# Kernel optimization log

Hardware: AMD Instinct MI355X
Metric: run time of the kernel (lower is better)

The kernel has to match this reference:

```python
import jax, jax.numpy as jnp
import numpy as np
from jax import lax

B, S, H, W = 8, 8, 256, 256  # batch, split_num, crop_size, crop_size


def _sn(w, seed):
    # spectral norm, 1 power iteration, u/v detached (torch spectral_norm semantics)
    o = w.shape[0]
    m = w.reshape(o, -1)
    u = jnp.asarray(np.random.RandomState(seed).randn(o).astype(np.float32))
    u = u / (jnp.linalg.norm(u) + 1e-12)
    v = m.T @ u
    v = v / (jnp.linalg.norm(v) + 1e-12)
    u2 = m @ v
    u2 = u2 / (jnp.linalg.norm(u2) + 1e-12)
    u2 = lax.stop_gradient(u2)
    v = lax.stop_gradient(v)
    sigma = u2 @ (m @ v)
    return w / sigma


def _conv(x, w, stride, groups):
    return lax.conv_general_dilated(x, w, (stride, stride), ((1, 1), (1, 1)),
                                    feature_group_count=groups,
                                    dimension_numbers=('NCHW', 'OIHW', 'NCHW'))


def _inorm(x):
    # InstanceNorm2d(affine=False, eps=1e-5)
    m = x.mean((2, 3), keepdims=True)
    v = ((x - m) ** 2).mean((2, 3), keepdims=True)
    return (x - m) * lax.rsqrt(v + 1e-5)


def _lrelu(x):
    return jnp.where(x >= 0, x, 0.2 * x)


def _crop_resize(img, mask):
    # img [3,H,W], mask [H,W]: mask, bbox of nonzero support, nearest-resize crop to (H,W)
    seg = img * mask
    c = seg.sum(0)
    col = c.sum(0)   # y_seg, per-column sums [W]
    row = c.sum(1)   # x_seg, per-row sums [H]
    cnz = col != 0
    rnz = row != 0
    ok = jnp.any(cnz) & jnp.any(rnz)
    y0 = jnp.argmax(cnz)
    y1 = W - 1 - jnp.argmax(cnz[::-1])
    x0 = jnp.argmax(rnz)
    x1 = H - 1 - jnp.argmax(rnz[::-1])
    h = x1 - x0 + 1
    w = y1 - y0 + 1
    # torch F.interpolate nearest: src = floor(dst * in / out)
    r = x0 + (jnp.arange(H) * h) // H
    cc = y0 + (jnp.arange(W) * w) // W
    resized = seg[:, r[:, None], cc[None, :]]
    return jnp.where(ok, resized, seg)


def _trans_img(real_image, semantic):
    f = jax.vmap(lambda img, masks: jax.vmap(lambda m: _crop_resize(img, m))(masks))
    imgs = f(real_image, semantic)            # [B,S,3,H,W]
    return imgs.reshape(B, S * 3, H, W)


def _forward(real_image, input_semantic, w1, w2, w3, w4, w5, w6, gw1, gb1, gw2, gb2):
    images = _trans_img(real_image, input_semantic)
    a = _lrelu
    x = _inorm(_conv(images, _sn(w1, 1), 2, S))          # [B,64,128,128]
    x = _inorm(_conv(a(x), _sn(w2, 2), 2, S))            # [B,128,64,64]
    out_8 = _inorm(_conv(a(x), _sn(w3, 3), 2, S))        # [B,256,32,32]
    out_16 = _inorm(_conv(a(out_8), _sn(w4, 4), 2, S))   # [B,512,16,16]
    out_32 = _inorm(_conv(a(out_16), _sn(w5, 5), 2, S))  # [B,1024,8,8]
    x = a(_inorm(_conv(a(out_32), _sn(w6, 6), 1, S)))    # [B,2048,8,8]
    x_1 = a(_conv(a(out_16), gw1, 1, 1) + gb1[None, :, None, None])  # [B,2048,16,16]
    x_2 = a(_conv(a(out_8), gw2, 1, 1) + gb2[None, :, None, None])   # [B,2048,32,32]
    return x, x_1, x_2, images


def setup_inputs() -> dict:
    key = jax.random.key(0)
    ks = jax.random.split(key, 12)
    real_image = jax.random.normal(ks[0], (B, 3, H, W), jnp.float32)
    input_semantic = jax.random.randint(ks[1], (B, S, H, W), 0, 2).astype(jnp.float32)
    def cw(k, o, i, kk=3):
        return jax.random.normal(k, (o, i, kk, kk), jnp.float32) * 0.05
    return {
        'real_image': real_image,
        'input_semantic': input_semantic,
        'w1': cw(ks[2], 64, 3),
        'w2': cw(ks[3], 128, 8),
        'w3': cw(ks[4], 256, 16),
        'w4': cw(ks[5], 512, 32),
        'w5': cw(ks[6], 1024, 64),
        'w6': cw(ks[7], 2048, 128),
        'gw1': cw(ks[8], 2048, 512, 1),
        'gb1': jnp.zeros((2048,), jnp.float32),
        'gw2': cw(ks[9], 2048, 256, 1),
        'gb2': jnp.zeros((2048,), jnp.float32),
    }


def reference(real_image, input_semantic, w1, w2, w3, w4, w5, w6, gw1, gb1, gw2, gb2):
    return _forward(real_image, input_semantic, w1, w2, w3, w4, w5, w6, gw1, gb1, gw2, gb2)
```

## Files before the change

kernel.cpp:

```cpp
#include <hip/hip_runtime.h>
#include <math.h>

#define WS_OFF_U     0
#define WS_OFF_T     4096
#define WS_OFF_TN    6400
#define WS_OFF_S2    6408
#define WS_OFF_BBOX  6416
#define WS_OFF_W     8192
#define WS_OFF_C     3152896
#define WS_OFF_D     5250048

#define OUT_X    0
#define OUT_X1   1048576
#define OUT_X2   6356992
#define OUT_IMG  25296896

struct Ptr6 { const float* p[6]; };

typedef short s16x8 __attribute__((ext_vector_type(8)));
typedef float f32x4 __attribute__((ext_vector_type(4)));
typedef unsigned int u32x4 __attribute__((ext_vector_type(4)));

#define MT_UP 0x80000000u
#define MT_LO 0x7fffffffu

__global__ __launch_bounds__(256) void gen_u_par(float* ws){
  const int os[6]   = {64,128,256,512,1024,2048};
  const int uoff[6] = {0,64,192,448,960,1984};
  int l = blockIdx.x;
  int n = os[l];
  int tid = threadIdx.x;

  __shared__ unsigned mt[624];
  __shared__ unsigned draws[8192];
  __shared__ float px[2048], py[2048];
  __shared__ unsigned char accf[2048];
  __shared__ int scan[256];

  if (tid == 0){
    unsigned seed = (unsigned)(l + 1);
    for (int i = 0; i < 624; i++){
      mt[i] = seed;
      seed = 1812433253u * (seed ^ (seed >> 30)) + (unsigned)(i + 1);
    }
  }
  __syncthreads();

  int need = 4 * n;
  int twists = (need + 623) / 624;
  for (int t = 0; t < twists; t++){
    unsigned yA = 0, vA = 0;
    if (tid < 227){ yA = (mt[tid] & MT_UP) | (mt[tid+1] & MT_LO); vA = mt[tid+397]; }
    __syncthreads();
    if (tid < 227){ mt[tid] = vA ^ (yA >> 1) ^ ((yA & 1u) ? 0x9908b0dfu : 0u); }
    __syncthreads();
    unsigned yB = 0, vB = 0; int iB = 227 + tid;
    if (tid < 227){ yB = (mt[iB] & MT_UP) | (mt[iB+1] & MT_LO); vB = mt[iB-227]; }
    __syncthreads();
    if (tid < 227){ mt[iB] = vB ^ (yB >> 1) ^ ((yB & 1u) ? 0x9908b0dfu : 0u); }
    __syncthreads();
    unsigned yC = 0, vC = 0; int iC = 454 + tid;
    if (tid < 169){ yC = (mt[iC] & MT_UP) | (mt[iC+1] & MT_LO); vC = mt[iC-227]; }
    __syncthreads();
    if (tid < 169){ mt[iC] = vC ^ (yC >> 1) ^ ((yC & 1u) ? 0x9908b0dfu : 0u); }
    __syncthreads();
    if (tid == 0){
      unsigned y = (mt[623] & MT_UP) | (mt[0] & MT_LO);
      mt[623] = mt[396] ^ (y >> 1) ^ ((y & 1u) ? 0x9908b0dfu : 0u);
    }
    __syncthreads();
    for (int i = tid; i < 624; i += 256){
      int pos = t * 624 + i;
      if (pos < need){
        unsigned y = mt[i];
        y ^= y >> 11; y ^= (y << 7) & 0x9d2c5680u; y ^= (y << 15) & 0xefc60000u; y ^= y >> 18;
        draws[pos] = y;
      }
    }
    __syncthreads();
  }

  int A = (n + 255) / 256;
  int local = 0;
  for (int a = 0; a < A; a++){
    int k = tid * A + a;
    if (k < n){
      double u1 = ((draws[4*k]   >> 5) * 67108864.0 + (draws[4*k+1] >> 6)) / 9007199254740992.0;
      double u2 = ((draws[4*k+2] >> 5) * 67108864.0 + (draws[4*k+3] >> 6)) / 9007199254740992.0;
      double x1 = 2.0*u1 - 1.0, x2 = 2.0*u2 - 1.0;
      double r2 = x1*x1 + x2*x2;
      int ok = (r2 < 1.0 && r2 != 0.0);
      accf[k] = (unsigned char)ok;
      if (ok){
        double f = sqrt(-2.0 * log(r2) / r2);
        px[k] = (float)(f * x2);
        py[k] = (float)(f * x1);
      }
      local += ok;
    }
  }
  scan[tid] = local;
  __syncthreads();
  if (tid == 0){
    int run = 0;
    for (int i = 0; i < 256; i++){ int c = scan[i]; scan[i] = run; run += c; }
  }
  __syncthreads();
  int j = scan[tid];
  float* u = ws + WS_OFF_U + uoff[l];
  for (int a = 0; a < A; a++){
    int k = tid * A + a;
    if (k < n && accf[k]){
      if (2*j + 1 < n){ u[2*j] = px[k]; u[2*j+1] = py[k]; }
      j++;
    }
  }
}

__global__ __launch_bounds__(256) void sn_t_kernel(Ptr6 wp, float* ws){
  const int cols[6] = {27,72,144,288,576,1152};
  const int uoff[6] = {0,64,192,448,960,1984};
  const int toff[6] = {0,27,99,243,531,1107};
  const int cstart[7] = {0,4,12,28,60,124,252};
  int b = blockIdx.x;
  int l = 0; while (l < 5 && b >= cstart[l+1]) l++;
  int chunk = b - cstart[l];
  int r0 = chunk * 16;
  int C = cols[l];
  const float* m = wp.p[l];
  const float* u = ws + WS_OFF_U + uoff[l];
  float* t = ws + WS_OFF_T + toff[l];
  __shared__ float us[16];
  if (threadIdx.x < 16) us[threadIdx.x] = u[r0 + threadIdx.x];
  __syncthreads();
  for (int j = threadIdx.x; j < C; j += 256){
    float acc = 0.f;
    #pragma unroll
    for (int r = 0; r < 16; r++) acc += m[(size_t)(r0 + r) * C + j] * us[r];
    atomicAdd(&t[j], acc);
  }
}

__global__ void sn_tn_kernel(float* ws){
  const int cols[6] = {27,72,144,288,576,1152};
  const int toff[6] = {0,27,99,243,531,1107};
  int l = blockIdx.x;
  const float* t = ws + WS_OFF_T + toff[l];
  float s = 0.f;
  for (int j = threadIdx.x; j < cols[l]; j += 256){ float v = t[j]; s += v*v; }
  __shared__ float sb[4];
  int lane = threadIdx.x & 63, wid = threadIdx.x >> 6;
  for (int o = 32; o; o >>= 1) s += __shfl_down(s, o, 64);
  if (lane == 0) sb[wid] = s;
  __syncthreads();
  if (threadIdx.x == 0) ws[WS_OFF_TN + l] = sb[0] + sb[1] + sb[2] + sb[3];
}

__global__ __launch_bounds__(256) void sn_z_kernel(Ptr6 wp, float* ws){
  const int cols[6] = {27,72,144,288,576,1152};
  const int toff[6] = {0,27,99,243,531,1107};
  const int rstart[7] = {0,64,192,448,960,1984,4032};
  __shared__ float part[6];
  if (threadIdx.x < 6) part[threadIdx.x] = 0.f;
  __syncthreads();
  int gr = blockIdx.x * 4 + (threadIdx.x >> 6);
  int lane = threadIdx.x & 63;
  if (gr < 4032){
    int l = 0; while (l < 5 && gr >= rstart[l+1]) l++;
    int row = gr - rstart[l];
    int C = cols[l];
    const float* m = wp.p[l] + (size_t)row * C;
    const float* t = ws + WS_OFF_T + toff[l];
    float acc = 0.f;
    for (int c = lane; c < C; c += 64) acc += m[c] * t[c];
    for (int o = 32; o; o >>= 1) acc += __shfl_down(acc, o, 64);
    if (lane == 0) atomicAdd(&part[l], acc * acc);
  }
  __syncthreads();
  if (threadIdx.x < 6 && part[threadIdx.x] != 0.f)
    atomicAdd(&ws[WS_OFF_S2 + threadIdx.x], part[threadIdx.x]);
}

__global__ void wscale_kernel(const float* __restrict__ src, float* __restrict__ dst,
                              int n, const float* __restrict__ tn, const float* __restrict__ s2){
  int i = blockIdx.x * 256 + threadIdx.x;
  if (i >= n) return;
  float inv = sqrtf(tn[0] / s2[0]);
  dst[i] = src[i] * inv;
}

__global__ __launch_bounds__(256) void bbox_stage1(const float* __restrict__ img,
                                                   const float* __restrict__ sem,
                                                   int* __restrict__ colpart,
                                                   int* __restrict__ rowflag){
  int chunk = blockIdx.x;
  int s = blockIdx.y;
  int b = blockIdx.z;
  int w = threadIdx.x;
  int h0 = chunk * 32;
  const float* i0 = img + (size_t)(b*3 + 0) * 65536;
  const float* i1 = i0 + 65536;
  const float* i2 = i1 + 65536;
  const float* mk = sem + (size_t)(b*8 + s) * 65536;
  __shared__ int rflags[32];
  if (w < 32) rflags[w] = 0;
  __syncthreads();
  int lane = w & 63;
  int myflag = 0;
  #pragma unroll 4
  for (int r = 0; r < 32; r++){
    int off = (h0 + r)*256 + w;
    float v = (i0[off] + i1[off] + i2[off]) * mk[off];
    int nz = (v != 0.f);
    myflag |= nz;
    unsigned long long bal = __ballot(nz);
    if (lane == 0 && bal) rflags[r] = 1;
  }
  __syncthreads();
  int bs = b*8 + s;
  colpart[(bs*8 + chunk)*256 + w] = myflag;
  if (w < 32) rowflag[bs*256 + h0 + w] = rflags[w];
}

__global__ __launch_bounds__(256) void bbox_stage2(const int* __restrict__ colpart,
                                                   const int* __restrict__ rowflag,
                                                   int* __restrict__ bbox){
  int bs = blockIdx.x;
  int w = threadIdx.x;
  int colnz = 0;
  #pragma unroll
  for (int c = 0; c < 8; c++) colnz |= colpart[(bs*8 + c)*256 + w];
  int rownz = rowflag[bs*256 + w];
  __shared__ int red[256];
  red[w] = colnz ? w : 256; __syncthreads();
  for (int st = 128; st; st >>= 1){ if (w < st) red[w] = min(red[w], red[w+st]); __syncthreads(); }
  int y0 = red[0]; __syncthreads();
  red[w] = colnz ? w : -1; __syncthreads();
  for (int st = 128; st; st >>= 1){ if (w < st) red[w] = max(red[w], red[w+st]); __syncthreads(); }
  int y1 = red[0]; __syncthreads();
  red[w] = rownz ? w : 256; __syncthreads();
  for (int st = 128; st; st >>= 1){ if (w < st) red[w] = min(red[w], red[w+st]); __syncthreads(); }
  int x0 = red[0]; __syncthreads();
  red[w] = rownz ? w : -1; __syncthreads();
  for (int st = 128; st; st >>= 1){ if (w < st) red[w] = max(red[w], red[w+st]); __syncthreads(); }
  int x1 = red[0];
  if (w == 0){
    int ok = (y0 < 256) && (x0 < 256);
    int base = bs * 4;
    bbox[base+0] = ok ? x0 : 0;
    bbox[base+1] = ok ? (x1 - x0 + 1) : 256;
    bbox[base+2] = ok ? y0 : 0;
    bbox[base+3] = ok ? (y1 - y0 + 1) : 256;
  }
}

__global__ void transimg_kernel(const float* __restrict__ img, const float* __restrict__ sem,
                                const int* __restrict__ bbox, float* __restrict__ out){
  int idx = blockIdx.x * 256 + threadIdx.x;
  int j = idx & 255;
  int i = (idx >> 8) & 255;
  int c = idx >> 16;
  int b = c / 24, ch24 = c % 24;
  int s = ch24 / 3, ch = ch24 % 3;
  const int* bb = bbox + (b*8 + s) * 4;
  int ri = bb[0] + ((i * bb[1]) >> 8);
  int cj = bb[2] + ((j * bb[3]) >> 8);
  float m = sem[((size_t)(b*8 + s) * 256 + ri) * 256 + cj];
  float v = img[((size_t)(b*3 + ch) * 256 + ri) * 256 + cj];
  out[idx] = v * m;
}

template<int CIN_G, int CIN_CHUNK, int COUT_G, int OCC, int RELU_IN>
__global__ __launch_bounds__(256) void conv3x3_tile(const float* __restrict__ in,
                                                    const float* __restrict__ wt,
                                                    float* __restrict__ out,
                                                    int Hin, int Hout){
  constexpr int TIH = 65, TIW = 65, RS = 66;
  constexpr int NOC = COUT_G / OCC;
  constexpr int NSTAGE = CIN_G / CIN_CHUNK;
  __shared__ float xs[CIN_CHUNK][TIH][RS];
  __shared__ float wsh[OCC][CIN_CHUNK*9];
  int tid = threadIdx.x;
  int g = blockIdx.y, b = blockIdx.z;
  int ocChunk = blockIdx.x % NOC;
  int tileId  = blockIdx.x / NOC;
  int tilesX = Hout >> 5;
  int tileX = tileId % tilesX, tileY = tileId / tilesX;
  int oh0 = tileY*32, ow0 = tileX*32;
  int ih0 = oh0*2 - 1, iw0 = ow0*2 - 1;
  int sx = tid & 15, sy = tid >> 4;
  const int Cin_tot = CIN_G*8;

  float acc[OCC][2][2];
  #pragma unroll
  for (int o = 0; o < OCC; o++)
    #pragma unroll
    for (int i2 = 0; i2 < 2; i2++)
      #pragma unroll
      for (int j2 = 0; j2 < 2; j2++) acc[o][i2][j2] = 0.f;

  for (int st = 0; st < NSTAGE; st++){
    int icb = st*CIN_CHUNK;
    for (int i = tid; i < CIN_CHUNK*TIH*TIW; i += 256){
      int ic = i / (TIH*TIW);
      int rem = i - ic*(TIH*TIW);
      int r = rem / TIW, c = rem - r*TIW;
      int ih = ih0 + r, iw = iw0 + c;
      float v = 0.f;
      if ((unsigned)ih < (unsigned)Hin && (unsigned)iw < (unsigned)Hin){
        v = in[((size_t)(b*Cin_tot + g*CIN_G + icb + ic)*Hin + ih)*Hin + iw];
        if (RELU_IN) v = (v >= 0.f) ? v : 0.2f*v;
      }
      xs[ic][r][c] = v;
    }
    for (int i = tid; i < OCC*CIN_CHUNK*9; i += 256){
      int o = i / (CIN_CHUNK*9);
      int rr = i - o*(CIN_CHUNK*9);
      int ic = rr / 9, tap = rr - ic*9;
      wsh[o][rr] = wt[((size_t)(g*COUT_G + ocChunk*OCC + o)*CIN_G + icb + ic)*9 + tap];
    }
    __syncthreads();
    #pragma unroll
    for (int ic = 0; ic < CIN_CHUNK; ic++){
      #pragma unroll
      for (int kh = 0; kh < 3; kh++){
        #pragma unroll
        for (int kw = 0; kw < 3; kw++){
          float wv[OCC];
          #pragma unroll
          for (int o = 0; o < OCC; o++) wv[o] = wsh[o][ic*9 + kh*3 + kw];
          #pragma unroll
          for (int i2 = 0; i2 < 2; i2++){
            #pragma unroll
            for (int j2 = 0; j2 < 2; j2++){
              float x = xs[ic][2*(sy + 16*i2) + kh][2*(sx + 16*j2) + kw];
              #pragma unroll
              for (int o = 0; o < OCC; o++) acc[o][i2][j2] += wv[o]*x;
            }
          }
        }
      }
    }
    if (st + 1 < NSTAGE) __syncthreads();
  }

  #pragma unroll
  for (int o = 0; o < OCC; o++){
    int oc = g*COUT_G + ocChunk*OCC + o;
    #pragma unroll
    for (int i2 = 0; i2 < 2; i2++)
      #pragma unroll
      for (int j2 = 0; j2 < 2; j2++){
        int oh = oh0 + sy + 16*i2, ow = ow0 + sx + 16*j2;
        out[((size_t)(b*COUT_G*8 + oc)*Hout + oh)*Hout + ow] = acc[o][i2][j2];
      }
  }
}

template<int STRIDE, int CIN_G, int COUT_G, int HSH>
__global__ __launch_bounds__(256) void conv3x3_gemm(const float* __restrict__ in,
                                                    const float* __restrict__ wt,
                                                    float* __restrict__ out,
                                                    int Hin){
  constexpr int K = CIN_G*9;
  const int Hout = 1 << HSH;
  int z = blockIdx.z; int b = z >> 3, g = z & 7;
  int n0 = blockIdx.x * 64, oc0 = blockIdx.y * 64;
  __shared__ float Ws[16][68];
  __shared__ float Xs[16][68];
  int tid = threadIdx.x;
  int tx = tid & 15, ty = tid >> 4;
  int pixl = tid & 63;
  int kkb = (tid >> 6) << 2;
  float acc[4][4];
  #pragma unroll
  for (int i = 0; i < 4; i++)
    #pragma unroll
    for (int j = 0; j < 4; j++) acc[i][j] = 0.f;

  for (int k0 = 0; k0 < K; k0 += 16){
    #pragma unroll
    for (int r = 0; r < 4; r++){
      int oc_l = (tid >> 4) + 16*r;
      int kk = tid & 15;
      Ws[kk][oc_l] = wt[((size_t)(g*COUT_G + oc0 + oc_l))*K + k0 + kk];
    }
    #pragma unroll
    for (int r = 0; r < 4; r++){
      int kk = kkb + r;
      int k = k0 + kk;
      int ic = k / 9, tap = k - ic*9;
      int dh = tap / 3, dw = tap - dh*3;
      int n = n0 + pixl;
      int oh = n >> HSH, ow = n & (Hout - 1);
      int ih = oh*STRIDE - 1 + dh, iw = ow*STRIDE - 1 + dw;
      float v = 0.f;
      if ((unsigned)ih < (unsigned)Hin && (unsigned)iw < (unsigned)Hin){
        v = in[((size_t)(b*CIN_G*8 + g*CIN_G + ic)*Hin + ih)*Hin + iw];
        v = (v >= 0.f) ? v : 0.2f*v;
      }
      Xs[kk][pixl] = v;
    }
    __syncthreads();
    #pragma unroll
    for (int kk = 0; kk < 16; kk++){
      float4 wv = *(const float4*)&Ws[kk][ty*4];
      float4 xv = *(const float4*)&Xs[kk][tx*4];
      acc[0][0] += wv.x*xv.x; acc[0][1] += wv.x*xv.y; acc[0][2] += wv.x*xv.z; acc[0][3] += wv.x*xv.w;
      acc[1][0] += wv.y*xv.x; acc[1][1] += wv.y*xv.y; acc[1][2] += wv.y*xv.z; acc[1][3] += wv.y*xv.w;
      acc[2][0] += wv.z*xv.x; acc[2][1] += wv.z*xv.y; acc[2][2] += wv.z*xv.z; acc[2][3] += wv.z*xv.w;
      acc[3][0] += wv.w*xv.x; acc[3][1] += wv.w*xv.y; acc[3][2] += wv.w*xv.z; acc[3][3] += wv.w*xv.w;
    }
    __syncthreads();
  }

  #pragma unroll
  for (int i = 0; i < 4; i++){
    int oc = g*COUT_G + oc0 + ty*4 + i;
    #pragma unroll
    for (int j = 0; j < 4; j++){
      int n = n0 + tx*4 + j;
      int oh = n >> HSH, ow = n & (Hout - 1);
      out[((size_t)(b*COUT_G*8 + oc)*Hout + oh)*Hout + ow] = acc[i][j];
    }
  }
}

__global__ void inorm_kernel(const float* __restrict__ in, float* __restrict__ out,
                             int N, int relu_out){
  int bc = blockIdx.x;
  const float* p = in + (size_t)bc * N;
  float* q = out + (size_t)bc * N;
  float s = 0.f, ss = 0.f;
  for (int i = threadIdx.x; i < N; i += blockDim.x){ float x = p[i]; s += x; ss += x*x; }
  __shared__ float sb[8];
  int lane = threadIdx.x & 63, wid = threadIdx.x >> 6;
  for (int o = 32; o; o >>= 1){ s += __shfl_down(s, o, 64); ss += __shfl_down(ss, o, 64); }
  if (lane == 0){ sb[wid] = s; sb[4 + wid] = ss; }
  __syncthreads();
  if (threadIdx.x == 0){
    int nw = blockDim.x >> 6;
    float S = 0.f, SS = 0.f;
    for (int i = 0; i < nw; i++){ S += sb[i]; SS += sb[4+i]; }
    float mean = S / N;
    float var = SS / N - mean*mean;
    sb[0] = mean;
    sb[4] = rsqrtf(var + 1e-5f);
  }
  __syncthreads();
  float mean = sb[0], r = sb[4];
  for (int i = threadIdx.x; i < N; i += blockDim.x){
    float y = (p[i] - mean) * r;
    if (relu_out) y = (y >= 0.f) ? y : 0.2f*y;
    q[i] = y;
  }
}

template<int P>
__global__ void inorm_sum(const float* __restrict__ in, float* __restrict__ out,
                          int N, size_t pstride, int relu_out){
  int bc = blockIdx.x;
  const float* p = in + (size_t)bc * N;
  float* q = out + (size_t)bc * N;
  float s = 0.f, ss = 0.f;
  for (int i = threadIdx.x; i < N; i += blockDim.x){
    float x = 0.f;
    #pragma unroll
    for (int pp = 0; pp < P; pp++) x += p[(size_t)pp*pstride + i];
    q[i] = x;
    s += x; ss += x*x;
  }
  __shared__ float sb[8];
  int lane = threadIdx.x & 63, wid = threadIdx.x >> 6;
  for (int o = 32; o; o >>= 1){ s += __shfl_down(s, o, 64); ss += __shfl_down(ss, o, 64); }
  if (lane == 0){ sb[wid] = s; sb[4 + wid] = ss; }
  __syncthreads();
  if (threadIdx.x == 0){
    int nw = blockDim.x >> 6;
    float S = 0.f, SS = 0.f;
    for (int i = 0; i < nw; i++){ S += sb[i]; SS += sb[4+i]; }
    float mean = S / N;
    float var = SS / N - mean*mean;
    sb[0] = mean;
    sb[4] = rsqrtf(var + 1e-5f);
  }
  __syncthreads();
  float mean = sb[0], r = sb[4];
  for (int i = threadIdx.x; i < N; i += blockDim.x){
    float y = (q[i] - mean) * r;
    if (relu_out) y = (y >= 0.f) ? y : 0.2f*y;
    q[i] = y;
  }
}

__device__ __forceinline__ void split_bf16(float v, unsigned short& h, unsigned short& l){
  unsigned u = __float_as_uint(v);
  unsigned r = (u + 0x7FFFu + ((u >> 16) & 1u)) >> 16;
  h = (unsigned short)r;
  float hf = __uint_as_float(r << 16);
  float lo = v - hf;
  unsigned u2 = __float_as_uint(lo);
  unsigned r2 = (u2 + 0x7FFFu + ((u2 >> 16) & 1u)) >> 16;
  l = (unsigned short)r2;
}

template<int C, int HW>
__global__ __launch_bounds__(256) void cvt_x_kernel(const float* __restrict__ src,
                                                    unsigned short* __restrict__ dst){
  __shared__ float tile[64][65];
  int b = blockIdx.z;
  int c0 = blockIdx.y * 64, p0 = blockIdx.x * 64;
  const float* sp = src + ((size_t)b*C + c0)*HW + p0;
  for (int i = threadIdx.x; i < 64*64; i += 256){
    int ch = i >> 6, px = i & 63;
    float v = sp[(size_t)ch*HW + px];
    tile[ch][px] = (v >= 0.f) ? v : 0.2f*v;
  }
  __syncthreads();
  unsigned short* dp = dst + ((size_t)b*HW + p0)*(3*C) + c0;
  for (int i = threadIdx.x; i < 64*64; i += 256){
    int px = i >> 6, ch = i & 63;
    float v = tile[ch][px];
    unsigned short h, l; split_bf16(v, h, l);
    unsigned short* row = dp + (size_t)px*(3*C);
    row[ch] = h; row[C + ch] = l; row[2*C + ch] = h;
  }
}

template<int C>
__global__ __launch_bounds__(256) void cvt_w_kernel(const float* __restrict__ wt,
                                                    unsigned short* __restrict__ dst){
  int i = blockIdx.x * 256 + threadIdx.x;
  int oc = i / C, k = i & (C - 1);
  float v = wt[i];
  unsigned short h, l; split_bf16(v, h, l);
  unsigned short* row = dst + (size_t)oc * 3 * C;
  row[k] = h; row[C + k] = h; row[2*C + k] = l;
}

template<int K>
__global__ __launch_bounds__(256) void cvt_w_g(const float* __restrict__ wt,
                                               unsigned short* __restrict__ dst, int total){
  int i = blockIdx.x * 256 + threadIdx.x;
  if (i >= total) return;
  int oc = i / K, k = i - oc*K;
  float v = wt[i];
  unsigned short h, l; split_bf16(v, h, l);
  unsigned short* row = dst + (size_t)oc * 3 * K;
  row[k] = h; row[K + k] = h; row[2*K + k] = l;
}

template<int K, int K3PAD>
__global__ __launch_bounds__(256) void cvt_w_pad(const float* __restrict__ wt,
                                                 unsigned short* __restrict__ dst, int total){
  int i = blockIdx.x * 256 + threadIdx.x;
  if (i >= total) return;
  int oc = i / K3PAD, kk = i - oc*K3PAD;
  unsigned short o = 0;
  if (kk < 3*K){
    int which = kk / K, k = kk - which*K;
    float v = wt[(size_t)oc*K + k];
    unsigned short h, l; split_bf16(v, h, l);
    o = (which == 2) ? l : h;
  }
  dst[i] = o;
}

template<int CIN_G, int Hin, int STRIDE>
__global__ __launch_bounds__(256) void cvt_im2col(const float* __restrict__ in,
                                                  unsigned short* __restrict__ dst){
  constexpr int K = CIN_G*9;
  constexpr int K3 = 3*K;
  int g = blockIdx.x, b = blockIdx.y, pc = blockIdx.z;
  const float* src = in + (size_t)(b*CIN_G*8 + g*CIN_G)*Hin*Hin;
  unsigned short* drow = dst + ((size_t)g*512 + b*64 + pc*16)*K3;
  for (int idx = threadIdx.x; idx < 16*K; idx += 256){
    int pixl = idx / K, k = idx - pixl*K;
    int ic = k / 9, tap = k - ic*9;
    int dh = tap / 3, dw = tap - dh*3;
    int gp = pc*16 + pixl;
    int oh = gp >> 3, ow = gp & 7;
    int ih = oh*STRIDE - 1 + dh, iw = ow*STRIDE - 1 + dw;
    float v = 0.f;
    if ((unsigned)ih < (unsigned)Hin && (unsigned)iw < (unsigned)Hin){
      v = src[((size_t)ic*Hin + ih)*Hin + iw];
      v = (v >= 0.f) ? v : 0.2f*v;
    }
    unsigned short h, l; split_bf16(v, h, l);
    unsigned short* row = drow + (size_t)pixl*K3;
    row[k] = h; row[K + k] = l; row[2*K + k] = h;
  }
}

template<int CIN_G, int Hin, int HOSH, int STRIDE, int K3PAD, int NB>
__global__ __launch_bounds__(256) void cvt_im2col_g(const float* __restrict__ in,
                                                    unsigned short* __restrict__ dst, int b0){
  constexpr int K = CIN_G*9;
  constexpr int Hout = 1 << HOSH;
  constexpr int HW = Hout*Hout;
  int g = blockIdx.x, bl = blockIdx.y, pc = blockIdx.z;
  int b = b0 + bl;
  const float* src = in + (size_t)(b*CIN_G*8 + g*CIN_G)*Hin*Hin;
  unsigned short* drow = dst + ((size_t)g*(NB*HW) + (size_t)bl*HW + pc*64)*K3PAD;
  for (int idx = threadIdx.x; idx < 64*K; idx += 256){
    int pixl = idx / K, k = idx - pixl*K;
    int ic = k / 9, tap = k - ic*9;
    int dh = tap / 3, dw = tap - dh*3;
    int gp = pc*64 + pixl;
    int oh = gp >> HOSH, ow = gp & (Hout - 1);
    int ih = oh*STRIDE - 1 + dh, iw = ow*STRIDE - 1 + dw;
    float v = 0.f;
    if ((unsigned)ih < (unsigned)Hin && (unsigned)iw < (unsigned)Hin){
      v = src[((size_t)ic*Hin + ih)*Hin + iw];
      v = (v >= 0.f) ? v : 0.2f*v;
    }
    unsigned short h, l; split_bf16(v, h, l);
    unsigned short* row = drow + (size_t)pixl*K3PAD;
    row[k] = h; row[K + k] = l; row[2*K + k] = h;
  }
  for (int idx = threadIdx.x; idx < 64*(K3PAD - 3*K); idx += 256){
    int pixl = idx / (K3PAD - 3*K), k = idx - pixl*(K3PAD - 3*K);
    drow[(size_t)pixl*K3PAD + 3*K + k] = 0;
  }
}

template<int K3, int HW, int H>
__global__ __launch_bounds__(256) void conv1x1_mfma(const unsigned short* __restrict__ XT,
                                                    const unsigned short* __restrict__ WT,
                                                    const float* __restrict__ bias,
                                                    float* __restrict__ out){
  constexpr int Wp = H + 2;
  constexpr int NKT = K3 / 64;
  __shared__ unsigned short As[8*128*8];
  __shared__ unsigned short Bs[8*128*8];
  int tid = threadIdx.x;
  int b = blockIdx.z;
  int oc0 = blockIdx.y * 128;
  int px0 = blockIdx.x * 128;
  int lane = tid & 63;
  int wv = tid >> 6;
  int wy = wv >> 1, wx = wv & 1;

  int srow = tid >> 3;
  int sc8  = tid & 7;
  const unsigned short* Ag = WT + (size_t)(oc0 + srow)*K3 + sc8*8;
  const unsigned short* Bg = XT + ((size_t)b*HW + px0 + srow)*K3 + sc8*8;

  f32x4 acc[4][4];
  #pragma unroll
  for (int i = 0; i < 4; i++)
    #pragma unroll
    for (int j = 0; j < 4; j++) acc[i][j] = (f32x4){0.f,0.f,0.f,0.f};

  for (int kt = 0; kt < NKT; kt++){
    int k0 = kt * 64;
    #pragma unroll
    for (int q = 0; q < 4; q++){
      u32x4 av = *(const u32x4*)(Ag + (size_t)(32*q)*K3 + k0);
      u32x4 bv = *(const u32x4*)(Bg + (size_t)(32*q)*K3 + k0);
      *(u32x4*)&As[(sc8*128 + srow + 32*q)*8] = av;
      *(u32x4*)&Bs[(sc8*128 + srow + 32*q)*8] = bv;
    }
    __syncthreads();
    #pragma unroll
    for (int s = 0; s < 2; s++){
      int cb = s*4 + (lane >> 4);
      s16x8 af[4], bfr[4];
      #pragma unroll
      for (int mt = 0; mt < 4; mt++)
        af[mt] = *(const s16x8*)&As[(cb*128 + wy*64 + mt*16 + (lane & 15))*8];
      #pragma unroll
      for (int nt = 0; nt < 4; nt++)
        bfr[nt] = *(const s16x8*)&Bs[(cb*128 + wx*64 + nt*16 + (lane & 15))*8];
      #pragma unroll
      for (int mt = 0; mt < 4; mt++)
        #pragma unroll
        for (int nt = 0; nt < 4; nt++)
          acc[mt][nt] = __builtin_amdgcn_mfma_f32_16x16x32_bf16(af[mt], bfr[nt], acc[mt][nt], 0, 0, 0);
    }
    __syncthreads();
  }

  #pragma unroll
  for (int mt = 0; mt < 4; mt++){
    #pragma unroll
    for (int r = 0; r < 4; r++){
      int oc = oc0 + wy*64 + mt*16 + (lane >> 4)*4 + r;
      float bv2 = bias[oc];
      float* ob = out + ((size_t)b*2048 + oc)*Wp*Wp;
      #pragma unroll
      for (int nt = 0; nt < 4; nt++){
        int pix = px0 + wx*64 + nt*16 + (lane & 15);
        int ph = pix / H, pw2 = pix % H;
        float v = acc[mt][nt][r] + bv2;
        v = (v >= 0.f) ? v : 0.2f*v;
        ob[(size_t)(ph + 1)*Wp + pw2 + 1] = v;
      }
    }
  }
}

template<int K3, int COUT_G, int CTOT, int KSPLIT>
__global__ __launch_bounds__(256) void grouped_mfma(const unsigned short* __restrict__ XT,
                                                    const unsigned short* __restrict__ WT,
                                                    float* __restrict__ out, size_t pstride){
  constexpr int NKT = K3 / 64;
  constexpr int SPK = NKT / KSPLIT;
  __shared__ unsigned short As[8*128*8];
  __shared__ unsigned short Bs[8*128*8];
  int tid = threadIdx.x;
  int oc0 = blockIdx.y * 128;
  int g = oc0 / COUT_G;
  int px0 = blockIdx.x * 128;
  int ks = blockIdx.z;
  out += (size_t)ks * pstride;
  int lane = tid & 63;
  int wv = tid >> 6;
  int wy = wv >> 1, wx = wv & 1;

  int srow = tid >> 3;
  int sc8  = tid & 7;
  const unsigned short* Ag = WT + (size_t)(oc0 + srow)*K3 + sc8*8;
  const unsigned short* Bg = XT + ((size_t)g*512 + px0 + srow)*K3 + sc8*8;

  f32x4 acc[4][4];
  #pragma unroll
  for (int i = 0; i < 4; i++)
    #pragma unroll
    for (int j = 0; j < 4; j++) acc[i][j] = (f32x4){0.f,0.f,0.f,0.f};

  for (int kt = ks*SPK; kt < (ks+1)*SPK; kt++){
    int k0 = kt * 64;
    #pragma unroll
    for (int q = 0; q < 4; q++){
      u32x4 av = *(const u32x4*)(Ag + (size_t)(32*q)*K3 + k0);
      u32x4 bv = *(const u32x4*)(Bg + (size_t)(32*q)*K3 + k0);
      int rr = srow + 32*q;
      *(u32x4*)&As[(sc8*128 + (rr ^ sc8))*8] = av;
      *(u32x4*)&Bs[(sc8*128 + (rr ^ sc8))*8] = bv;
    }
    __syncthreads();
    #pragma unroll
    for (int s = 0; s < 2; s++){
      int cb = s*4 + (lane >> 4);
      s16x8 af[4], bfr[4];
      #pragma unroll
      for (int mt = 0; mt < 4; mt++){
        int row = wy*64 + mt*16 + (lane & 15);
        af[mt] = *(const s16x8*)&As[(cb*128 + (row ^ cb))*8];
      }
      #pragma unroll
      for (int nt = 0; nt < 4; nt++){
        int row = wx*64 + nt*16 + (lane & 15);
        bfr[nt] = *(const s16x8*)&Bs[(cb*128 + (row ^ cb))*8];
      }
      #pragma unroll
      for (int mt = 0; mt < 4; mt++)
        #pragma unroll
        for (int nt = 0; nt < 4; nt++)
          acc[mt][nt] = __builtin_amdgcn_mfma_f32_16x16x32_bf16(af[mt], bfr[nt], acc[mt][nt], 0, 0, 0);
    }
    __syncthreads();
  }

  #pragma unroll
  for (int mt = 0; mt < 4; mt++){
    #pragma unroll
    for (int r = 0; r < 4; r++){
      int oc = oc0 + wy*64 + mt*16 + (lane >> 4)*4 + r;
      #pragma unroll
      for (int nt = 0; nt < 4; nt++){
        int row = px0 + wx*64 + nt*16 + (lane & 15);
        int b = row >> 6, p = row & 63;
        out[((size_t)(b*CTOT + oc))*64 + p] = acc[mt][nt][r];
      }
    }
  }
}

template<int K3PAD, int COUT_G, int CTOT, int HW, int NROWS>
__global__ __launch_bounds__(256) void gconv_mfma(const unsigned short* __restrict__ XT,
                                                  const unsigned short* __restrict__ WT,
                                                  float* __restrict__ out, int b0){
  constexpr int NKT = K3PAD / 64;
  constexpr int MF = COUT_G / 16;
  __shared__ unsigned short As[8*COUT_G*8];
  __shared__ unsigned short Bs[8*128*8];
  int tid = threadIdx.x;
  int g = blockIdx.y;
  int px0 = blockIdx.x * 128;
  int lane = tid & 63;
  int wv = tid >> 6;

  int srow = tid >> 3;
  int sc8  = tid & 7;
  const unsigned short* Ag = WT + (size_t)(g*COUT_G + (srow & (COUT_G-1)))*K3PAD + sc8*8;
  const unsigned short* Bg = XT + ((size_t)g*NROWS + px0 + srow)*K3PAD + sc8*8;

  f32x4 acc[MF][2];
  #pragma unroll
  for (int i = 0; i < MF; i++)
    #pragma unroll
    for (int j = 0; j < 2; j++) acc[i][j] = (f32x4){0.f,0.f,0.f,0.f};

  for (int kt = 0; kt < NKT; kt++){
    int k0 = kt * 64;
    if (srow < COUT_G)
      *(u32x4*)&As[(sc8*COUT_G + srow)*8] = *(const u32x4*)(Ag + k0);
    #pragma unroll
    for (int q = 0; q < 4; q++)
      *(u32x4*)&Bs[(sc8*128 + srow + 32*q)*8] = *(const u32x4*)(Bg + (size_t)(32*q)*K3PAD + k0);
    __syncthreads();
    #pragma unroll
    for (int s = 0; s < 2; s++){
      int cb = s*4 + (lane >> 4);
      s16x8 af[MF], bfr[2];
      #pragma unroll
      for (int mt = 0; mt < MF; mt++)
        af[mt] = *(const s16x8*)&As[(cb*COUT_G + mt*16 + (lane & 15))*8];
      #pragma unroll
      for (int nt = 0; nt < 2; nt++)
        bfr[nt] = *(const s16x8*)&Bs[(cb*128 + wv*32 + nt*16 + (lane & 15))*8];
      #pragma unroll
      for (int mt = 0; mt < MF; mt++)
        #pragma unroll
        for (int nt = 0; nt < 2; nt++)
          acc[mt][nt] = __builtin_amdgcn_mfma_f32_16x16x32_bf16(af[mt], bfr[nt], acc[mt][nt], 0, 0, 0);
    }
    __syncthreads();
  }

  #pragma unroll
  for (int mt = 0; mt < MF; mt++){
    #pragma unroll
    for (int r = 0; r < 4; r++){
      int oc = g*COUT_G + mt*16 + (lane >> 4)*4 + r;
      #pragma unroll
      for (int nt = 0; nt < 2; nt++){
        int rowg = px0 + wv*32 + nt*16 + (lane & 15);
        int bl = rowg / HW, px = rowg - bl*HW;
        out[((size_t)((b0 + bl)*CTOT + oc))*HW + px] = acc[mt][nt][r];
      }
    }
  }
}

__global__ void border_kernel(const float* __restrict__ bias, float* __restrict__ out, int H){
  int Wp = H + 2, perim = 4*Wp - 4;
  int p = threadIdx.x;
  if (p >= perim) return;
  int oc = blockIdx.y, b = blockIdx.z;
  int ph, pw;
  if (p < Wp){ ph = 0; pw = p; }
  else if (p < 2*Wp){ ph = Wp - 1; pw = p - Wp; }
  else { int q = p - 2*Wp; ph = 1 + (q >> 1); pw = (q & 1) ? (Wp - 1) : 0; }
  float bv = bias[oc];
  bv = (bv >= 0.f) ? bv : 0.2f*bv;
  out[(((size_t)b*2048 + oc)*Wp + ph)*Wp + pw] = bv;
}

extern "C" void kernel_launch(void* const* d_in, const int* in_sizes, int n_in,
                              void* d_out, int out_size, void* d_ws, size_t ws_size,
                              hipStream_t stream){
  const float* img = (const float*)d_in[0];
  const float* sem = (const float*)d_in[1];
  Ptr6 wp;
  for (int l = 0; l < 6; l++) wp.p[l] = (const float*)d_in[2 + l];
  const float* gw1 = (const float*)d_in[8];
  const float* gb1 = (const float*)d_in[9];
  const float* gw2 = (const float*)d_in[10];
  const float* gb2 = (const float*)d_in[11];
  float* out = (float*)d_out;
  float* ws  = (float*)d_ws;

  float* bufA = out + OUT_X2;
  float* bufB = bufA + 8388608;
  float* bufC = ws + WS_OFF_C;
  float* bufD = ws + WS_OFF_D;
  int* bbox = (int*)(ws + WS_OFF_BBOX);
  int* colpart = (int*)(bufB + 8388608);
  int* rowflag = colpart + 64*8*256;

  unsigned short* XT2 = (unsigned short*)(out + OUT_X1);
  unsigned short* W2  = (unsigned short*)(out + OUT_X1 + 3145728);
  unsigned short* XT1 = (unsigned short*)(ws + WS_OFF_W);
  unsigned short* W1  = (unsigned short*)(ws + WS_OFF_W + 1572864);

  unsigned short* XT5 = (unsigned short*)(bufA + 1048576);
  unsigned short* W5s = (unsigned short*)(bufB);
  unsigned short* XT6 = (unsigned short*)(bufA + 1048576);
  unsigned short* W6s = (unsigned short*)(bufB + 1048576);

  unsigned short* X3i = (unsigned short*)bufA;
  unsigned short* W3s = (unsigned short*)(bufB + 8388608);
  float* out3raw = out + OUT_X1;

  static const int kWOff[6]  = {0,1728,10944,47808,195264,785088};
  static const int kWSize[6] = {1728,9216,36864,147456,589824,2359296};

  hipMemsetAsync(ws + WS_OFF_T, 0, (WS_OFF_S2 + 8 - WS_OFF_T) * sizeof(float), stream);

  gen_u_par<<<6, 256, 0, stream>>>(ws);
  sn_t_kernel<<<252, 256, 0, stream>>>(wp, ws);
  sn_tn_kernel<<<6, 256, 0, stream>>>(ws);
  sn_z_kernel<<<1008, 256, 0, stream>>>(wp, ws);
  for (int l = 0; l < 6; l++)
    wscale_kernel<<<(kWSize[l]+255)/256, 256, 0, stream>>>(wp.p[l], ws + WS_OFF_W + kWOff[l],
                                                           kWSize[l], ws + WS_OFF_TN + l, ws + WS_OFF_S2 + l);

  bbox_stage1<<<dim3(8,8,8), 256, 0, stream>>>(img, sem, colpart, rowflag);
  bbox_stage2<<<64, 256, 0, stream>>>(colpart, rowflag, bbox);
  transimg_kernel<<<49152, 256, 0, stream>>>(img, sem, bbox, out + OUT_IMG);

  conv3x3_tile<3,3,8,8,0><<<dim3(16,8,8), 256, 0, stream>>>(out + OUT_IMG, ws + WS_OFF_W + kWOff[0],
                                                            bufA, 256, 128);
  inorm_kernel<<<512, 256, 0, stream>>>(bufA, bufB, 16384, 0);
  conv3x3_tile<8,2,16,16,1><<<dim3(4,8,8), 256, 0, stream>>>(bufB, ws + WS_OFF_W + kWOff[1],
                                                             bufA, 128, 64);
  inorm_kernel<<<1024, 256, 0, stream>>>(bufA, bufB, 4096, 0);

  cvt_w_pad<144,448><<<(256*448+255)/256, 256, 0, stream>>>(ws + WS_OFF_W + kWOff[2], W3s, 256*448);
  for (int s = 0; s < 2; s++){
    cvt_im2col_g<16,64,5,2,448,4><<<dim3(8,4,16), 256, 0, stream>>>(bufB, X3i, 4*s);
    gconv_mfma<448,32,256,1024,4096><<<dim3(32,8), 256, 0, stream>>>(X3i, W3s, out3raw, 4*s);
  }
  inorm_kernel<<<2048, 256, 0, stream>>>(out3raw, bufC, 1024, 0);

  conv3x3_gemm<2,32,64,4><<<dim3(4,1,64), 256, 0, stream>>>(bufC, ws + WS_OFF_W + kWOff[3], bufA, 32);
  inorm_kernel<<<4096, 256, 0, stream>>>(bufA, bufD, 256, 0);

  cvt_im2col<64,16,2><<<dim3(8,8,4), 256, 0, stream>>>(bufD, XT5);
  cvt_w_g<576><<<2304, 256, 0, stream>>>(ws + WS_OFF_W + kWOff[4], W5s, 589824);
  grouped_mfma<1728,128,1024,3><<<dim3(4,8,3), 256, 0, stream>>>(XT5, W5s, out + OUT_X1, 524288);
  inorm_sum<3><<<8192, 64, 0, stream>>>(out + OUT_X1, bufB, 64, 524288, 0);

  cvt_im2col<128,8,1><<<dim3(8,8,4), 256, 0, stream>>>(bufB, XT6);
  cvt_w_g<1152><<<9216, 256, 0, stream>>>(ws + WS_OFF_W + kWOff[5], W6s, 2359296);
  grouped_mfma<3456,256,2048,6><<<dim3(4,16,6), 256, 0, stream>>>(XT6, W6s, out, 1048576);
  inorm_sum<6><<<16384, 64, 0, stream>>>(out, out + OUT_X, 64, 1048576, 1);

  cvt_x_kernel<256,1024><<<dim3(16,4,8), 256, 0, stream>>>(bufC, XT2);
  cvt_w_kernel<256><<<2048, 256, 0, stream>>>(gw2, W2);
  cvt_x_kernel<512,256><<<dim3(4,8,8), 256, 0, stream>>>(bufD, XT1);
  cvt_w_kernel<512><<<4096, 256, 0, stream>>>(gw1, W1);

  border_kernel<<<dim3(1,2048,8), 256, 0, stream>>>(gb2, out + OUT_X2, 32);
  conv1x1_mfma<768,1024,32><<<dim3(8,16,8), 256, 0, stream>>>(XT2, W2, gb2, out + OUT_X2);
  border_kernel<<<dim3(1,2048,8), 256, 0, stream>>>(gb1, out + OUT_X1, 16);
  conv1x1_mfma<1536,256,16><<<dim3(2,16,8), 256, 0, stream>>>(XT1, W1, gb1, out + OUT_X1);
}
```

Baseline: 677.6 us.

## Move layer-2 grouped conv to bf16 MFMA GEMM and swizzle LDS tiles

Layer 2's grouped 3x3 conv was a direct FP32 tiled kernel. It now runs as a bf16 im2col plus grouped MFMA GEMM, processed in four batch chunks, with a padded bf16 weight conversion. Separately, the GEMM kernel's LDS tile indexing is XOR-swizzled by k-chunk to reduce shared-memory bank conflicts on fragment loads. This adds extra launches and im2col traffic, and lowers the precision of layer 2 to bf16.

```diff
diff --git a/kernel.cpp b/kernel.cpp
--- a/kernel.cpp
+++ b/kernel.cpp
@@ -806,21 +806,27 @@
   for (int kt = 0; kt < NKT; kt++){
     int k0 = kt * 64;
     if (srow < COUT_G)
-      *(u32x4*)&As[(sc8*COUT_G + srow)*8] = *(const u32x4*)(Ag + k0);
-    #pragma unroll
-    for (int q = 0; q < 4; q++)
-      *(u32x4*)&Bs[(sc8*128 + srow + 32*q)*8] = *(const u32x4*)(Bg + (size_t)(32*q)*K3PAD + k0);
+      *(u32x4*)&As[(sc8*COUT_G + (srow ^ sc8))*8] = *(const u32x4*)(Ag + k0);
+    #pragma unroll
+    for (int q = 0; q < 4; q++){
+      int rr = srow + 32*q;
+      *(u32x4*)&Bs[(sc8*128 + (rr ^ sc8))*8] = *(const u32x4*)(Bg + (size_t)(32*q)*K3PAD + k0);
+    }
     __syncthreads();
     #pragma unroll
     for (int s = 0; s < 2; s++){
       int cb = s*4 + (lane >> 4);
       s16x8 af[MF], bfr[2];
       #pragma unroll
-      for (int mt = 0; mt < MF; mt++)
-        af[mt] = *(const s16x8*)&As[(cb*COUT_G + mt*16 + (lane & 15))*8];
-      #pragma unroll
-      for (int nt = 0; nt < 2; nt++)
-        bfr[nt] = *(const s16x8*)&Bs[(cb*128 + wv*32 + nt*16 + (lane & 15))*8];
+      for (int mt = 0; mt < MF; mt++){
+        int row = mt*16 + (lane & 15);
+        af[mt] = *(const s16x8*)&As[(cb*COUT_G + (row ^ cb))*8];
+      }
+      #pragma unroll
+      for (int nt = 0; nt < 2; nt++){
+        int row = wv*32 + nt*16 + (lane & 15);
+        bfr[nt] = *(const s16x8*)&Bs[(cb*128 + (row ^ cb))*8];
+      }
       #pragma unroll
       for (int mt = 0; mt < MF; mt++)
         #pragma unroll
@@ -895,6 +901,10 @@
   unsigned short* W3s = (unsigned short*)(bufB + 8388608);
   float* out3raw = out + OUT_X1;
 
+  unsigned short* X2i = (unsigned short*)bufA;
+  unsigned short* W2s = (unsigned short*)(bufB + 8388608 + 57344);
+  float* out2raw = out + OUT_X1;
+
   static const int kWOff[6]  = {0,1728,10944,47808,195264,785088};
   static const int kWSize[6] = {1728,9216,36864,147456,589824,2359296};
 
@@ -915,9 +925,13 @@
   conv3x3_tile<3,3,8,8,0><<<dim3(16,8,8), 256, 0, stream>>>(out + OUT_IMG, ws + WS_OFF_W + kWOff[0],
                                                             bufA, 256, 128);
   inorm_kernel<<<512, 256, 0, stream>>>(bufA, bufB, 16384, 0);
-  conv3x3_tile<8,2,16,16,1><<<dim3(4,8,8), 256, 0, stream>>>(bufB, ws + WS_OFF_W + kWOff[1],
-                                                             bufA, 128, 64);
-  inorm_kernel<<<1024, 256, 0, stream>>>(bufA, bufB, 4096, 0);
+
+  cvt_w_pad<72,256><<<(128*256+255)/256, 256, 0, stream>>>(ws + WS_OFF_W + kWOff[1], W2s, 128*256);
+  for (int s = 0; s < 4; s++){
+    cvt_im2col_g<8,128,6,2,256,2><<<dim3(8,2,64), 256, 0, stream>>>(bufB, X2i, 2*s);
+    gconv_mfma<256,16,128,4096,8192><<<dim3(64,8), 256, 0, stream>>>(X2i, W2s, out2raw, 2*s);
+  }
+  inorm_kernel<<<1024, 256, 0, stream>>>(out2raw, bufB, 4096, 0);
 
   cvt_w_pad<144,448><<<(256*448+255)/256, 256, 0, stream>>>(ws + WS_OFF_W + kWOff[2], W3s, 256*448);
   for (int s = 0; s < 2; s++){
```

Measured after the change: 671.7 us. No clear change (-0.9%).
